# Kernel tuning notes

Hardware: AMD Instinct MI355X
Metric: run time of the kernel (lower is better)

The kernel has to match this reference:

```python
import jax, jax.numpy as jnp
import numpy as np

EMBED_DIM = 1024
NUM_HEADS = 16
HEAD_DIM = EMBED_DIM // NUM_HEADS


def setup_inputs() -> dict:
    key = jax.random.key(0)
    ks = jax.random.split(key, 9)
    B, S, D = 2, 2048, EMBED_DIM
    scale = 1.0 / np.sqrt(D)
    x = jax.random.normal(ks[0], (B, S, D), dtype=jnp.float32)
    # Linear params (torch nn.Linear: y = x @ W.T + b); store W as [out, in]
    Wq = jax.random.normal(ks[1], (D, D), dtype=jnp.float32) * scale
    bq = jnp.zeros((D,), dtype=jnp.float32)
    Wk = jax.random.normal(ks[2], (D, D), dtype=jnp.float32) * scale
    bk = jnp.zeros((D,), dtype=jnp.float32)
    Wv = jax.random.normal(ks[3], (D, D), dtype=jnp.float32) * scale
    bv = jnp.zeros((D,), dtype=jnp.float32)
    Wo = jax.random.normal(ks[4], (D, D), dtype=jnp.float32) * scale
    bo = jnp.zeros((D,), dtype=jnp.float32)
    return {"x": x, "Wq": Wq, "bq": bq, "Wk": Wk, "bk": bk,
            "Wv": Wv, "bv": bv, "Wo": Wo, "bo": bo}


def reference(x, Wq, bq, Wk, bk, Wv, bv, Wo, bo):
    B, S, D = x.shape
    H, Hd = NUM_HEADS, HEAD_DIM
    scaling = Hd ** -0.5
    # projections (torch Linear: x @ W.T + b)
    q = (x @ Wq.T + bq).reshape(B, S, H, Hd).transpose(0, 2, 1, 3)  # [B,H,S,Hd]
    k = (x @ Wk.T + bk).reshape(B, S, H, Hd).transpose(0, 2, 1, 3)
    v = (x @ Wv.T + bv).reshape(B, S, H, Hd).transpose(0, 2, 1, 3)
    # full score matrix, as in the original (no flash tiling)
    scores = jnp.einsum('bhqd,bhkd->bhqk', q, k) * scaling  # [B,H,S,S]
    attn = jax.nn.softmax(scores, axis=-1)
    # dropout is identity in eval mode
    out = jnp.einsum('bhqk,bhkd->bhqd', attn, v)  # [B,H,S,Hd]
    out = out.transpose(0, 2, 1, 3).reshape(B, S, D)
    return out @ Wo.T + bo
```

## Files before the change

### kernel.cpp

```cpp
#include <hip/hip_runtime.h>
#include <stdint.h>

typedef unsigned short u16;
typedef short short8 __attribute__((ext_vector_type(8)));
typedef float f32x4 __attribute__((ext_vector_type(4)));
typedef float f32x16 __attribute__((ext_vector_type(16)));
typedef float f32x2 __attribute__((ext_vector_type(2)));

__device__ __forceinline__ u16 f2bf_fast(float f) {
  union { float f; uint32_t u; } x;
  x.f = f;
  return (u16)((x.u + 0x8000u) >> 16);
}

__device__ __forceinline__ uint32_t pack2bf(float lo, float hi) {
  union { float f; uint32_t u; } a, b;
  a.f = lo; b.f = hi;
  return __builtin_amdgcn_perm(b.u + 0x8000u, a.u + 0x8000u, 0x07060302u);
}

__device__ __forceinline__ float bf2f(uint32_t u) {
  union { uint32_t u; float f; } x;
  x.u = u << 16;
  return x.f;
}

__device__ __forceinline__ uint32_t cvtpk(float lo, float hi) {
  uint32_t r;
  asm("v_cvt_pk_bf16_f32 %0, %1, %2" : "=v"(r) : "v"(lo), "v"(hi));
  return r;
}

__device__ __forceinline__ void permswap(uint32_t& a, uint32_t& b) {
  asm("v_permlane32_swap_b32 %0, %1" : "+v"(a), "+v"(b));
}

__device__ __forceinline__ void gload_lds16(const void* g, void* l) {
  __builtin_amdgcn_global_load_lds(
      (const __attribute__((address_space(1))) void*)g,
      (__attribute__((address_space(3))) void*)l, 16, 0, 0);
}

__device__ __forceinline__ f32x4 mfma16(short8 a, short8 b, f32x4 c) {
  return __builtin_amdgcn_mfma_f32_16x16x32_bf16(a, b, c, 0, 0, 0);
}

__device__ __forceinline__ f32x16 mfma32(short8 a, short8 b, f32x16 c) {
  return __builtin_amdgcn_mfma_f32_32x32x16_bf16(a, b, c, 0, 0, 0);
}

#define QSCALE 0.18033688011112042f

__global__ void pack_all(const float* __restrict__ x, const float* __restrict__ wq,
                         const float* __restrict__ wk, const float* __restrict__ wv,
                         const float* __restrict__ wo, u16* __restrict__ xp,
                         u16* __restrict__ wp) {
  const int gi = blockIdx.x * 256 + threadIdx.x;
  const int lane = gi & 63;
  const int kc = (gi >> 6) & 31;
  const int rt = gi >> 11;
  const int col = kc * 32 + (lane >> 4) * 8;
  const float* src;
  int row;
  if (rt < 256) {
    src = x;
    row = rt * 16 + (lane & 15);
  } else {
    const int wti = rt - 256;
    const int widx = wti >> 6;
    src = (widx == 0) ? wq : (widx == 1) ? wk : (widx == 2) ? wv : wo;
    row = (wti & 63) * 16 + (lane & 15);
  }
  const float4* p = (const float4*)(src + (size_t)row * 1024 + col);
  const float4 v0 = p[0], v1 = p[1];
  uint4 o;
  o.x = pack2bf(v0.x, v0.y);
  o.y = pack2bf(v0.z, v0.w);
  o.z = pack2bf(v1.x, v1.y);
  o.w = pack2bf(v1.z, v1.w);
  u16* dst = (rt < 256) ? xp : wp;
  const int og = (rt < 256) ? gi : gi - 524288;
  ((uint4*)dst)[og] = o;
}

__global__ __launch_bounds__(256, 3) void proj_qkv(
    const u16* __restrict__ xp, const u16* __restrict__ wp,
    const float* __restrict__ bq, const float* __restrict__ bk,
    const float* __restrict__ bv, u16* __restrict__ qw, u16* __restrict__ kw,
    u16* __restrict__ vw) {
  __shared__ __align__(16) u16 As[8192];
  __shared__ __align__(16) u16 Bs[8192];
  const int tid = threadIdx.x, lane = tid & 63, w = tid >> 6;
  const int quad = lane >> 4, l15 = lane & 15;

  const int bid = blockIdx.x;
  const int work = (bid & 7) * 96 + (bid >> 3);
  const bool isQK = work < 512;
  int at0, bt0, bm2, bn2;
  const u16 *Ap, *Bp;
  if (isQK) {
    bm2 = work >> 4; bn2 = work & 15;
    Ap = xp; at0 = bm2 * 8;
    Bp = wp; bt0 = bn2 * 8;
  } else {
    const int h = work - 512;
    bm2 = h >> 5; bn2 = h & 31;
    Ap = wp; at0 = 128 + bm2 * 8;
    Bp = xp; bt0 = bn2 * 8;
  }
  const int wr = w >> 1, wc = w & 1;
  const int bm = bm2 * 2 + wr, bn = bn2 * 2 + wc;

  f32x4 acc[4][4] = {};

  for (int ks = 0; ks < 16; ++ks) {
    const int kc0 = ks * 2;
#pragma unroll
    for (int i = 0; i < 8; ++i) {
      const int g = w * 8 + i;
      const int gg = g & 15, t = gg >> 1, c = gg & 1;
      const u16* src = (g < 16)
          ? (Ap + ((((at0 + t) << 5) + kc0 + c) * 64 + lane) * 8)
          : (Bp + ((((bt0 + t) << 5) + kc0 + c) * 64 + lane) * 8);
      u16* dst = ((g < 16) ? As : Bs) + (gg * 64 + lane) * 8;
      gload_lds16(src, dst);
    }
    __syncthreads();

    short8 af[4][2], bf[4][2];
#pragma unroll
    for (int mt = 0; mt < 4; ++mt)
#pragma unroll
      for (int c = 0; c < 2; ++c)
        af[mt][c] = *(const short8*)&As[((((wr * 4 + mt) << 1) + c) * 64 + lane) * 8];
#pragma unroll
    for (int nt = 0; nt < 4; ++nt)
#pragma unroll
      for (int c = 0; c < 2; ++c)
        bf[nt][c] = *(const short8*)&Bs[((((wc * 4 + nt) << 1) + c) * 64 + lane) * 8];

#pragma unroll
    for (int c = 0; c < 2; ++c)
#pragma unroll
      for (int mt = 0; mt < 4; ++mt)
#pragma unroll
        for (int nt = 0; nt < 4; ++nt)
          acc[mt][nt] = mfma16(af[mt][c], bf[nt][c], acc[mt][nt]);
    __syncthreads();
  }

#pragma unroll
  for (int nt = 0; nt < 4; ++nt) {
    const int n = bn * 64 + nt * 16 + l15;
#pragma unroll
    for (int mt = 0; mt < 4; ++mt)
#pragma unroll
      for (int r = 0; r < 4; ++r) {
        const int m = bm * 64 + mt * 16 + quad * 4 + r;
        const float a = acc[mt][nt][r];
        if (isQK) {
          const bool isQ = (bn < 16);
          const int nn = isQ ? n : n - 1024;
          const float v = isQ ? (a + bq[nn]) * QSCALE : a + bk[nn];
          u16* op = isQ ? qw : kw;
          const int b = m >> 11, s = m & 2047, hh = nn >> 6, d = nn & 63;
          op[((size_t)((b * 16 + hh) * 2048 + s)) * 64 + d] = f2bf_fast(v);
        } else {
          const float v = a + bv[m];
          const int b = n >> 11, s = n & 2047;
          vw[((size_t)(b * 1024 + m)) * 2048 + s] = f2bf_fast(v);
        }
      }
  }
}

__global__ __launch_bounds__(256, 4) void attn_kernel(
    const u16* __restrict__ Q, const u16* __restrict__ Kt,
    const u16* __restrict__ Vt, u16* __restrict__ op0, u16* __restrict__ op1,
    float* __restrict__ lp) {
  __shared__ __align__(16) u16 Sm[16384];
  const int tid = threadIdx.x, lane = tid & 63, w = tid >> 6;
  const int l31 = lane & 31, hi = lane >> 5, l7 = lane & 7;
  const int qt = blockIdx.x;
  const int bh = blockIdx.y >> 1;
  const int ks = blockIdx.y & 1;

  const char* Qb = (const char*)(Q + ((size_t)bh * 2048 + qt * 128) * 64);
  const char* Kb = (const char*)(Kt + ((size_t)bh * 2048 + ks * 1024) * 64);
  const char* Vb = (const char*)(Vt + (size_t)bh * 64 * 2048 + ks * 1024);

  auto stageKV = [&](int kt, int b) {
    u16* Kl = Sm + b * 4096;
    u16* Vl = Sm + 8192 + b * 4096;
#pragma unroll
    for (int i = 0; i < 2; ++i) {
      const int G = (w * 2 + i) * 64 + lane;
      const int r = G >> 3, sl = G & 7;
      gload_lds16(Kb + (size_t)(kt * 64 + r) * 128 + ((sl ^ (r & 7)) * 16),
                  &Kl[G * 8]);
      gload_lds16(Vb + (size_t)r * 4096 + kt * 128 + ((sl ^ (r & 7)) * 16),
                  &Vl[G * 8]);
    }
  };

#pragma unroll
  for (int i = 0; i < 4; ++i) {
    const int G = (w * 4 + i) * 64 + lane;
    const int row = G >> 3, sl = G & 7;
    u16* qdst = (G < 512) ? (Sm + 4096) : (Sm + 12288);
    gload_lds16(Qb + (size_t)row * 128 + ((sl ^ (row & 7)) * 16),
                &qdst[(G & 511) * 8]);
  }
  stageKV(0, 0);
  __syncthreads();

  const u16* qreg = (w < 2) ? (Sm + 4096) : (Sm + 12288);
  const int qr0 = (w & 1) * 32;
  short8 aq[4];
#pragma unroll
  for (int ds = 0; ds < 4; ++ds)
    aq[ds] = *(const short8*)&qreg[(qr0 + l31) * 64 + (((ds << 1) + hi) ^ l7) * 8];
  __syncthreads();

  f32x16 ot[2] = {};
  f32x2 l2 = {0.f, 0.f};

  for (int kt = 0; kt < 16; ++kt) {
    const int buf = kt & 1;
    if (kt < 15) stageKV(kt + 1, buf ^ 1);
    const u16* Kl = Sm + buf * 4096;
    const u16* Vl = Sm + 8192 + buf * 4096;

#pragma unroll
    for (int t = 0; t < 2; ++t) {
      f32x16 st = {};
#pragma unroll
      for (int ds = 0; ds < 4; ++ds) {
        short8 kf = *(const short8*)&Kl[(t * 32 + l31) * 64 +
                                        (((ds << 1) + hi) ^ l7) * 8];
        st = mfma32(kf, aq[ds], st);
      }
      float e[16];
#pragma unroll
      for (int i = 0; i < 16; ++i) e[i] = __builtin_amdgcn_exp2f(st[i]);
#pragma unroll
      for (int i = 0; i < 8; ++i) l2 += (f32x2){e[2 * i], e[2 * i + 1]};

      uint32_t p01 = cvtpk(e[0], e[1]),   p23 = cvtpk(e[2], e[3]);
      uint32_t p45 = cvtpk(e[4], e[5]),   p67 = cvtpk(e[6], e[7]);
      uint32_t p89 = cvtpk(e[8], e[9]),   pAB = cvtpk(e[10], e[11]);
      uint32_t pCD = cvtpk(e[12], e[13]), pEF = cvtpk(e[14], e[15]);
      permswap(p01, p45);
      permswap(p23, p67);
      permswap(p89, pCD);
      permswap(pAB, pEF);
      union { uint32_t u[4]; short8 s; } b0, b1;
      b0.u[0] = p01; b0.u[1] = p23; b0.u[2] = p45; b0.u[3] = p67;
      b1.u[0] = p89; b1.u[1] = pAB; b1.u[2] = pCD; b1.u[3] = pEF;

#pragma unroll
      for (int dt = 0; dt < 2; ++dt) {
#pragma unroll
        for (int s2 = 0; s2 < 2; ++s2) {
          short8 vf = *(const short8*)&Vl[(dt * 32 + l31) * 64 +
                                          ((((t * 2 + s2) << 1) + hi) ^ l7) * 8];
          ot[dt] = mfma32(vf, s2 ? b1.s : b0.s, ot[dt]);
        }
      }
    }
    if (kt < 15) __syncthreads();
  }

  const int b = bh >> 4, h = bh & 15;
  u16* op = ks ? op1 : op0;
  float l = l2.x + l2.y;
  l += __shfl_xor(l, 32);
  const int srow = qt * 128 + w * 32 + l31;
  if (hi == 0) lp[((size_t)(ks * 32 + bh)) * 2048 + srow] = l;
  const int rt = b * 128 + qt * 8 + w * 2 + (l31 >> 4);
#pragma unroll
  for (int dt = 0; dt < 2; ++dt) {
    const int kc = h * 2 + dt;
#pragma unroll
    for (int g = 0; g < 4; ++g) {
      const int ln = (lane & 15) + 16 * g;
      uint2 ov;
      ov.x = cvtpk(ot[dt][4 * g + 0], ot[dt][4 * g + 1]);
      ov.y = cvtpk(ot[dt][4 * g + 2], ot[dt][4 * g + 3]);
      *(uint2*)(op + ((size_t)((rt * 32 + kc) * 64 + ln)) * 8 + hi * 4) = ov;
    }
  }
}

__global__ void attn_combine(const u16* __restrict__ op0,
                             const u16* __restrict__ op1,
                             const float* __restrict__ lp,
                             u16* __restrict__ awp) {
  const int g = blockIdx.x * 256 + threadIdx.x;
  const int ln = g & 63;
  const int kc = (g >> 6) & 31;
  const int rt = g >> 11;
  const int row = rt * 16 + (ln & 15);
  const int b = row >> 11, s = row & 2047;
  const int h = kc >> 1;
  const int lidx = (b * 16 + h) * 2048 + s;
  const float inv = __builtin_amdgcn_rcpf(lp[lidx] + lp[lidx + 65536]);
  const uint4 a0 = ((const uint4*)op0)[g];
  const uint4 a1 = ((const uint4*)op1)[g];
  uint4 o;
  o.x = pack2bf((bf2f(a0.x) + bf2f(a1.x)) * inv,
                (bf2f(a0.x >> 16) + bf2f(a1.x >> 16)) * inv);
  o.y = pack2bf((bf2f(a0.y) + bf2f(a1.y)) * inv,
                (bf2f(a0.y >> 16) + bf2f(a1.y >> 16)) * inv);
  o.z = pack2bf((bf2f(a0.z) + bf2f(a1.z)) * inv,
                (bf2f(a0.z >> 16) + bf2f(a1.z >> 16)) * inv);
  o.w = pack2bf((bf2f(a0.w) + bf2f(a1.w)) * inv,
                (bf2f(a0.w >> 16) + bf2f(a1.w >> 16)) * inv);
  ((uint4*)awp)[g] = o;
}

__global__ __launch_bounds__(512, 2) void out_proj(const u16* __restrict__ awp,
                                                   const u16* __restrict__ wp,
                                                   const float* __restrict__ bo,
                                                   float* __restrict__ out) {
  __shared__ __align__(16) u16 As[8192];
  __shared__ __align__(16) u16 Bs[8192];
  const int tid = threadIdx.x, lane = tid & 63, w = tid >> 6;
  const int quad = lane >> 4, l15 = lane & 15;

  const int bid = blockIdx.x;
  const int work = (bid & 7) * 32 + (bid >> 3);
  const int bm2 = work >> 3, bn2 = work & 7;
  const int at0 = bm2 * 8, bt0 = 192 + bn2 * 8;
  const int wr = w >> 2, wc = w & 3;

  f32x4 acc[4][2] = {};

  for (int ks = 0; ks < 16; ++ks) {
    const int kc0 = ks * 2;
#pragma unroll
    for (int i = 0; i < 4; ++i) {
      const int g = w * 4 + i;
      const int gg = g & 15, t = gg >> 1, c = gg & 1;
      const u16* src = (g < 16)
          ? (awp + ((((at0 + t) << 5) + kc0 + c) * 64 + lane) * 8)
          : (wp + ((((bt0 + t) << 5) + kc0 + c) * 64 + lane) * 8);
      u16* dst = ((g < 16) ? As : Bs) + (gg * 64 + lane) * 8;
      gload_lds16(src, dst);
    }
    __syncthreads();

    short8 af[4][2], bf[2][2];
#pragma unroll
    for (int mt = 0; mt < 4; ++mt)
#pragma unroll
      for (int c = 0; c < 2; ++c)
        af[mt][c] = *(const short8*)&As[((((wr * 4 + mt) << 1) + c) * 64 + lane) * 8];
#pragma unroll
    for (int nt = 0; nt < 2; ++nt)
#pragma unroll
      for (int c = 0; c < 2; ++c)
        bf[nt][c] = *(const short8*)&Bs[((((wc * 2 + nt) << 1) + c) * 64 + lane) * 8];

#pragma unroll
    for (int c = 0; c < 2; ++c)
#pragma unroll
      for (int mt = 0; mt < 4; ++mt)
#pragma unroll
        for (int nt = 0; nt < 2; ++nt)
          acc[mt][nt] = mfma16(af[mt][c], bf[nt][c], acc[mt][nt]);
    __syncthreads();
  }

#pragma unroll
  for (int nt = 0; nt < 2; ++nt) {
    const int n = bn2 * 128 + wc * 32 + nt * 16 + l15;
    const float bb = bo[n];
#pragma unroll
    for (int mt = 0; mt < 4; ++mt)
#pragma unroll
      for (int r = 0; r < 4; ++r) {
        const int m = bm2 * 128 + wr * 64 + mt * 16 + quad * 4 + r;
        out[(size_t)m * 1024 + n] = acc[mt][nt][r] + bb;
      }
  }
}

extern "C" void kernel_launch(void* const* d_in, const int* in_sizes, int n_in,
                              void* d_out, int out_size, void* d_ws, size_t ws_size,
                              hipStream_t stream) {
  const float* x  = (const float*)d_in[0];
  const float* Wq = (const float*)d_in[1];
  const float* bq = (const float*)d_in[2];
  const float* Wk = (const float*)d_in[3];
  const float* bk = (const float*)d_in[4];
  const float* Wv = (const float*)d_in[5];
  const float* bv = (const float*)d_in[6];
  const float* Wo = (const float*)d_in[7];
  const float* bo = (const float*)d_in[8];

  const size_t M4 = (size_t)4 * 1024 * 1024;
  u16* xp  = (u16*)d_ws;
  u16* wp  = xp + M4;
  u16* qw  = wp + M4;
  u16* kw  = qw + M4;
  u16* vw  = kw + M4;
  u16* op1 = vw + M4;
  u16* awp = op1 + M4;
  float* lp = (float*)(awp + M4);
  u16* op0 = xp;

  pack_all<<<4096, 256, 0, stream>>>(x, Wq, Wk, Wv, Wo, xp, wp);

  proj_qkv<<<768, 256, 0, stream>>>(xp, wp, bq, bk, bv, qw, kw, vw);

  attn_kernel<<<dim3(16, 64), 256, 0, stream>>>(qw, kw, vw, op0, op1, lp);

  attn_combine<<<2048, 256, 0, stream>>>(op0, op1, lp, awp);

  out_proj<<<256, 512, 0, stream>>>(awp, wp, bo, (float*)d_out);
}
```

Baseline: 192.9 us.

## Double-buffer GEMM k-loops, drop attention key split and combine kernel

The QKV and output projection GEMMs now double-buffer one k-chunk at a time in LDS, so the next global-to-LDS load overlaps the current MFMAs instead of loading and then waiting each step. The attention kernel no longer splits keys into two halves. Each block processes all 32 key tiles and normalises by the row sum itself, which removes the separate combine kernel and its partial-output traffic. Priority hints are added around the MFMA sections. The cost is half as many attention blocks (512), which lowers parallelism and occupancy, and a doubled serial loop per block.

```diff
diff --git a/kernel.cpp b/kernel.cpp
--- a/kernel.cpp
+++ b/kernel.cpp
@@ -111,41 +111,43 @@
   const int wr = w >> 1, wc = w & 1;
   const int bm = bm2 * 2 + wr, bn = bn2 * 2 + wc;
 
+  auto stage = [&](int kc, int buf) {
+#pragma unroll
+    for (int i = 0; i < 4; ++i) {
+      const int g = w * 4 + i;
+      const int t = g & 7;
+      const u16* src = (g < 8)
+          ? (Ap + (((at0 + t) << 5) + kc) * 512 + lane * 8)
+          : (Bp + (((bt0 + t) << 5) + kc) * 512 + lane * 8);
+      u16* dst = ((g < 8) ? As : Bs) + (buf * 8 + t) * 512 + lane * 8;
+      gload_lds16(src, dst);
+    }
+  };
+
   f32x4 acc[4][4] = {};
 
-  for (int ks = 0; ks < 16; ++ks) {
-    const int kc0 = ks * 2;
-#pragma unroll
-    for (int i = 0; i < 8; ++i) {
-      const int g = w * 8 + i;
-      const int gg = g & 15, t = gg >> 1, c = gg & 1;
-      const u16* src = (g < 16)
-          ? (Ap + ((((at0 + t) << 5) + kc0 + c) * 64 + lane) * 8)
-          : (Bp + ((((bt0 + t) << 5) + kc0 + c) * 64 + lane) * 8);
-      u16* dst = ((g < 16) ? As : Bs) + (gg * 64 + lane) * 8;
-      gload_lds16(src, dst);
-    }
-    __syncthreads();
-
-    short8 af[4][2], bf[4][2];
-#pragma unroll
-    for (int mt = 0; mt < 4; ++mt)
-#pragma unroll
-      for (int c = 0; c < 2; ++c)
-        af[mt][c] = *(const short8*)&As[((((wr * 4 + mt) << 1) + c) * 64 + lane) * 8];
+  stage(0, 0);
+  __syncthreads();
+
+  for (int kc = 0; kc < 32; ++kc) {
+    const int cur = kc & 1;
+    if (kc < 31) stage(kc + 1, cur ^ 1);
+
+    const u16* Ab = As + cur * 4096;
+    const u16* Bb = Bs + cur * 4096;
+    short8 af[4], bf[4];
+#pragma unroll
+    for (int mt = 0; mt < 4; ++mt)
+      af[mt] = *(const short8*)&Ab[((wr * 4 + mt) * 64 + lane) * 8];
 #pragma unroll
     for (int nt = 0; nt < 4; ++nt)
-#pragma unroll
-      for (int c = 0; c < 2; ++c)
-        bf[nt][c] = *(const short8*)&Bs[((((wc * 4 + nt) << 1) + c) * 64 + lane) * 8];
-
-#pragma unroll
-    for (int c = 0; c < 2; ++c)
-#pragma unroll
-      for (int mt = 0; mt < 4; ++mt)
-#pragma unroll
-        for (int nt = 0; nt < 4; ++nt)
-          acc[mt][nt] = mfma16(af[mt][c], bf[nt][c], acc[mt][nt]);
+      bf[nt] = *(const short8*)&Bb[((wc * 4 + nt) * 64 + lane) * 8];
+
+#pragma unroll
+    for (int mt = 0; mt < 4; ++mt)
+#pragma unroll
+      for (int nt = 0; nt < 4; ++nt)
+        acc[mt][nt] = mfma16(af[mt], bf[nt], acc[mt][nt]);
     __syncthreads();
   }
 
@@ -176,18 +178,16 @@
 
 __global__ __launch_bounds__(256, 4) void attn_kernel(
     const u16* __restrict__ Q, const u16* __restrict__ Kt,
-    const u16* __restrict__ Vt, u16* __restrict__ op0, u16* __restrict__ op1,
-    float* __restrict__ lp) {
+    const u16* __restrict__ Vt, u16* __restrict__ awp) {
   __shared__ __align__(16) u16 Sm[16384];
   const int tid = threadIdx.x, lane = tid & 63, w = tid >> 6;
   const int l31 = lane & 31, hi = lane >> 5, l7 = lane & 7;
   const int qt = blockIdx.x;
-  const int bh = blockIdx.y >> 1;
-  const int ks = blockIdx.y & 1;
+  const int bh = blockIdx.y;
 
   const char* Qb = (const char*)(Q + ((size_t)bh * 2048 + qt * 128) * 64);
-  const char* Kb = (const char*)(Kt + ((size_t)bh * 2048 + ks * 1024) * 64);
-  const char* Vb = (const char*)(Vt + (size_t)bh * 64 * 2048 + ks * 1024);
+  const char* Kb = (const char*)(Kt + (size_t)bh * 2048 * 64);
+  const char* Vb = (const char*)(Vt + (size_t)bh * 64 * 2048);
 
   auto stageKV = [&](int kt, int b) {
     u16* Kl = Sm + b * 4096;
@@ -225,21 +225,23 @@
   f32x16 ot[2] = {};
   f32x2 l2 = {0.f, 0.f};
 
-  for (int kt = 0; kt < 16; ++kt) {
+  for (int kt = 0; kt < 32; ++kt) {
     const int buf = kt & 1;
-    if (kt < 15) stageKV(kt + 1, buf ^ 1);
+    if (kt < 31) stageKV(kt + 1, buf ^ 1);
     const u16* Kl = Sm + buf * 4096;
     const u16* Vl = Sm + 8192 + buf * 4096;
 
 #pragma unroll
     for (int t = 0; t < 2; ++t) {
       f32x16 st = {};
+      __builtin_amdgcn_s_setprio(1);
 #pragma unroll
       for (int ds = 0; ds < 4; ++ds) {
         short8 kf = *(const short8*)&Kl[(t * 32 + l31) * 64 +
                                         (((ds << 1) + hi) ^ l7) * 8];
         st = mfma32(kf, aq[ds], st);
       }
+      __builtin_amdgcn_s_setprio(0);
       float e[16];
 #pragma unroll
       for (int i = 0; i < 16; ++i) e[i] = __builtin_amdgcn_exp2f(st[i]);
@@ -258,6 +260,7 @@
       b0.u[0] = p01; b0.u[1] = p23; b0.u[2] = p45; b0.u[3] = p67;
       b1.u[0] = p89; b1.u[1] = pAB; b1.u[2] = pCD; b1.u[3] = pEF;
 
+      __builtin_amdgcn_s_setprio(1);
 #pragma unroll
       for (int dt = 0; dt < 2; ++dt) {
 #pragma unroll
@@ -267,16 +270,15 @@
           ot[dt] = mfma32(vf, s2 ? b1.s : b0.s, ot[dt]);
         }
       }
-    }
-    if (kt < 15) __syncthreads();
+      __builtin_amdgcn_s_setprio(0);
+    }
+    if (kt < 31) __syncthreads();
   }
 
   const int b = bh >> 4, h = bh & 15;
-  u16* op = ks ? op1 : op0;
   float l = l2.x + l2.y;
   l += __shfl_xor(l, 32);
-  const int srow = qt * 128 + w * 32 + l31;
-  if (hi == 0) lp[((size_t)(ks * 32 + bh)) * 2048 + srow] = l;
+  const float inv = __builtin_amdgcn_rcpf(l);
   const int rt = b * 128 + qt * 8 + w * 2 + (l31 >> 4);
 #pragma unroll
   for (int dt = 0; dt < 2; ++dt) {
@@ -285,38 +287,11 @@
     for (int g = 0; g < 4; ++g) {
       const int ln = (lane & 15) + 16 * g;
       uint2 ov;
-      ov.x = cvtpk(ot[dt][4 * g + 0], ot[dt][4 * g + 1]);
-      ov.y = cvtpk(ot[dt][4 * g + 2], ot[dt][4 * g + 3]);
-      *(uint2*)(op + ((size_t)((rt * 32 + kc) * 64 + ln)) * 8 + hi * 4) = ov;
-    }
-  }
-}
-
-__global__ void attn_combine(const u16* __restrict__ op0,
-                             const u16* __restrict__ op1,
-                             const float* __restrict__ lp,
-                             u16* __restrict__ awp) {
-  const int g = blockIdx.x * 256 + threadIdx.x;
-  const int ln = g & 63;
-  const int kc = (g >> 6) & 31;
-  const int rt = g >> 11;
-  const int row = rt * 16 + (ln & 15);
-  const int b = row >> 11, s = row & 2047;
-  const int h = kc >> 1;
-  const int lidx = (b * 16 + h) * 2048 + s;
-  const float inv = __builtin_amdgcn_rcpf(lp[lidx] + lp[lidx + 65536]);
-  const uint4 a0 = ((const uint4*)op0)[g];
-  const uint4 a1 = ((const uint4*)op1)[g];
-  uint4 o;
-  o.x = pack2bf((bf2f(a0.x) + bf2f(a1.x)) * inv,
-                (bf2f(a0.x >> 16) + bf2f(a1.x >> 16)) * inv);
-  o.y = pack2bf((bf2f(a0.y) + bf2f(a1.y)) * inv,
-                (bf2f(a0.y >> 16) + bf2f(a1.y >> 16)) * inv);
-  o.z = pack2bf((bf2f(a0.z) + bf2f(a1.z)) * inv,
-                (bf2f(a0.z >> 16) + bf2f(a1.z >> 16)) * inv);
-  o.w = pack2bf((bf2f(a0.w) + bf2f(a1.w)) * inv,
-                (bf2f(a0.w >> 16) + bf2f(a1.w >> 16)) * inv);
-  ((uint4*)awp)[g] = o;
+      ov.x = cvtpk(ot[dt][4 * g + 0] * inv, ot[dt][4 * g + 1] * inv);
+      ov.y = cvtpk(ot[dt][4 * g + 2] * inv, ot[dt][4 * g + 3] * inv);
+      *(uint2*)(awp + ((size_t)((rt * 32 + kc) * 64 + ln)) * 8 + hi * 4) = ov;
+    }
+  }
 }
 
 __global__ __launch_bounds__(512, 2) void out_proj(const u16* __restrict__ awp,
@@ -334,41 +309,43 @@
   const int at0 = bm2 * 8, bt0 = 192 + bn2 * 8;
   const int wr = w >> 2, wc = w & 3;
 
+  auto stage = [&](int kc, int buf) {
+#pragma unroll
+    for (int i = 0; i < 2; ++i) {
+      const int g = w * 2 + i;
+      const int t = g & 7;
+      const u16* src = (g < 8)
+          ? (awp + (((at0 + t) << 5) + kc) * 512 + lane * 8)
+          : (wp + (((bt0 + t) << 5) + kc) * 512 + lane * 8);
+      u16* dst = ((g < 8) ? As : Bs) + (buf * 8 + t) * 512 + lane * 8;
+      gload_lds16(src, dst);
+    }
+  };
+
   f32x4 acc[4][2] = {};
 
-  for (int ks = 0; ks < 16; ++ks) {
-    const int kc0 = ks * 2;
-#pragma unroll
-    for (int i = 0; i < 4; ++i) {
-      const int g = w * 4 + i;
-      const int gg = g & 15, t = gg >> 1, c = gg & 1;
-      const u16* src = (g < 16)
-          ? (awp + ((((at0 + t) << 5) + kc0 + c) * 64 + lane) * 8)
-          : (wp + ((((bt0 + t) << 5) + kc0 + c) * 64 + lane) * 8);
-      u16* dst = ((g < 16) ? As : Bs) + (gg * 64 + lane) * 8;
-      gload_lds16(src, dst);
-    }
-    __syncthreads();
-
-    short8 af[4][2], bf[2][2];
-#pragma unroll
-    for (int mt = 0; mt < 4; ++mt)
-#pragma unroll
-      for (int c = 0; c < 2; ++c)
-        af[mt][c] = *(const short8*)&As[((((wr * 4 + mt) << 1) + c) * 64 + lane) * 8];
+  stage(0, 0);
+  __syncthreads();
+
+  for (int kc = 0; kc < 32; ++kc) {
+    const int cur = kc & 1;
+    if (kc < 31) stage(kc + 1, cur ^ 1);
+
+    const u16* Ab = As + cur * 4096;
+    const u16* Bb = Bs + cur * 4096;
+    short8 af[4], bf[2];
+#pragma unroll
+    for (int mt = 0; mt < 4; ++mt)
+      af[mt] = *(const short8*)&Ab[((wr * 4 + mt) * 64 + lane) * 8];
 #pragma unroll
     for (int nt = 0; nt < 2; ++nt)
-#pragma unroll
-      for (int c = 0; c < 2; ++c)
-        bf[nt][c] = *(const short8*)&Bs[((((wc * 2 + nt) << 1) + c) * 64 + lane) * 8];
-
-#pragma unroll
-    for (int c = 0; c < 2; ++c)
-#pragma unroll
-      for (int mt = 0; mt < 4; ++mt)
-#pragma unroll
-        for (int nt = 0; nt < 2; ++nt)
-          acc[mt][nt] = mfma16(af[mt][c], bf[nt][c], acc[mt][nt]);
+      bf[nt] = *(const short8*)&Bb[((wc * 2 + nt) * 64 + lane) * 8];
+
+#pragma unroll
+    for (int mt = 0; mt < 4; ++mt)
+#pragma unroll
+      for (int nt = 0; nt < 2; ++nt)
+        acc[mt][nt] = mfma16(af[mt], bf[nt], acc[mt][nt]);
     __syncthreads();
   }
 
@@ -405,18 +382,13 @@
   u16* qw  = wp + M4;
   u16* kw  = qw + M4;
   u16* vw  = kw + M4;
-  u16* op1 = vw + M4;
-  u16* awp = op1 + M4;
-  float* lp = (float*)(awp + M4);
-  u16* op0 = xp;
+  u16* awp = vw + M4;
 
   pack_all<<<4096, 256, 0, stream>>>(x, Wq, Wk, Wv, Wo, xp, wp);
 
   proj_qkv<<<768, 256, 0, stream>>>(xp, wp, bq, bk, bv, qw, kw, vw);
 
-  attn_kernel<<<dim3(16, 64), 256, 0, stream>>>(qw, kw, vw, op0, op1, lp);
-
-  attn_combine<<<2048, 256, 0, stream>>>(op0, op1, lp, awp);
+  attn_kernel<<<dim3(16, 32), 256, 0, stream>>>(qw, kw, vw, awp);
 
   out_proj<<<256, 512, 0, stream>>>(awp, wp, bo, (float*)d_out);
 }
```

Measured after the change: 187.6 us. 2.8% less time.
